# Optimization experiments

Hardware: AMD Instinct MI355X
Metric: run time of the kernel (lower is better)

Reference implementation:

```python
import jax, jax.numpy as jnp
import numpy as np

R = 32          # voxel grid resolution (dense occupancy)
WIN = 8         # window_size
H = 16          # num_heads
C = 1024        # channels
D = C // H      # head_dim = 64
FREQ_DIM = D // 2 // 3   # 10 (3D rope)
ROPE_BASE = 10000.0
EPS_NORM = 1e-12


def setup_inputs() -> dict:
    key = jax.random.key(0)
    ks = jax.random.split(key, 4)
    N = R * R * R
    x = jax.random.normal(ks[0], (N, C), dtype=jnp.float32)
    # dense voxel grid coords in raster (x-major) order, matching token order
    gx, gy, gz = jnp.meshgrid(jnp.arange(R), jnp.arange(R), jnp.arange(R), indexing='ij')
    coords = jnp.stack([gx.reshape(-1), gy.reshape(-1), gz.reshape(-1)], axis=-1).astype(jnp.int32)
    Wqkv = jax.random.normal(ks[1], (C, 3 * C), dtype=jnp.float32) * 0.02
    bqkv = jnp.zeros((3 * C,), dtype=jnp.float32)
    gamma_q = jnp.ones((H, D), dtype=jnp.float32)
    gamma_k = jnp.ones((H, D), dtype=jnp.float32)
    Wout = jax.random.normal(ks[2], (C, C), dtype=jnp.float32) * 0.02
    bout = jnp.zeros((C,), dtype=jnp.float32)
    return {"x": x, "coords": coords, "Wqkv": Wqkv, "bqkv": bqkv,
            "gamma_q": gamma_q, "gamma_k": gamma_k, "Wout": Wout, "bout": bout}


def _mh_rms_norm(t, gamma):
    # SparseMultiHeadRMSNorm: fp32 F.normalize(dim=-1) * gamma * sqrt(D)
    tf = t.astype(jnp.float32)
    norm = jnp.maximum(jnp.sqrt(jnp.sum(tf * tf, axis=-1, keepdims=True)), EPS_NORM)
    return ((tf / norm) * gamma * (D ** 0.5)).astype(t.dtype)


def _rope_cos_sin(coords):
    # freqs: 1.0 / 10000**(i/freq_dim), i in [0, freq_dim)
    freqs = 1.0 / ROPE_BASE ** (jnp.arange(FREQ_DIM, dtype=jnp.float32) / FREQ_DIM)
    phases = coords.astype(jnp.float32)[:, :, None] * freqs  # [N, 3, FREQ_DIM]
    phases = phases.reshape(coords.shape[0], -1)             # [N, 30]
    pad = D // 2 - phases.shape[-1]
    phases = jnp.concatenate([phases, jnp.zeros((coords.shape[0], pad), jnp.float32)], axis=-1)
    return jnp.cos(phases), jnp.sin(phases)                  # [N, D//2] each


def _apply_rope(t, cos, sin):
    # t: [N, H, D] -> pairs [N, H, D//2, 2]; complex mult by (cos + i sin)
    tp = t.reshape(t.shape[0], H, D // 2, 2)
    t0, t1 = tp[..., 0], tp[..., 1]
    c = cos[:, None, :]
    s = sin[:, None, :]
    r0 = t0 * c - t1 * s
    r1 = t0 * s + t1 * c
    return jnp.stack([r0, r1], axis=-1).reshape(t.shape).astype(t.dtype)


def _to_windows(t):
    Rw = R // WIN
    t = t.reshape(Rw, WIN, Rw, WIN, Rw, WIN, H, D)
    t = t.transpose(0, 2, 4, 1, 3, 5, 6, 7)
    return t.reshape(Rw * Rw * Rw, WIN ** 3, H, D)


def _from_windows(t):
    Rw = R // WIN
    t = t.reshape(Rw, Rw, Rw, WIN, WIN, WIN, H, D)
    t = t.transpose(0, 3, 1, 4, 2, 5, 6, 7)
    return t.reshape(R * R * R, H, D)


def reference(x, coords, Wqkv, bqkv, gamma_q, gamma_k, Wout, bout):
    N = x.shape[0]
    qkv = (x @ Wqkv + bqkv).reshape(N, 3, H, D)
    q, k, v = qkv[:, 0], qkv[:, 1], qkv[:, 2]
    # per-head QK RMSNorm (before rope, as in forward)
    q = _mh_rms_norm(q, gamma_q)
    k = _mh_rms_norm(k, gamma_k)
    # inline 3D RoPE from voxel coords
    cos, sin = _rope_cos_sin(coords)
    q = _apply_rope(q, cos, sin)
    k = _apply_rope(k, cos, sin)
    # windowed self-attention (shift_window = (0,0,0), dense grid -> exact partition)
    qw, kw, vw = _to_windows(q), _to_windows(k), _to_windows(v)
    scale = 1.0 / (D ** 0.5)
    scores = jnp.einsum('wqhd,wkhd->whqk', qw, kw) * scale   # [nw, H, T, T]
    attn = jax.nn.softmax(scores, axis=-1)
    hw = jnp.einsum('whqk,wkhd->wqhd', attn, vw)
    h = _from_windows(hw).reshape(N, C)
    return h @ Wout + bout
```

## Files before the change

### kernel.cpp

```cpp
#include <hip/hip_runtime.h>
#include <hip/hip_bf16.h>
#include <stdint.h>

#define DEV static __device__ __forceinline__

typedef __attribute__((ext_vector_type(4))) float f32x4;
typedef __attribute__((ext_vector_type(8))) short s16x8;
typedef __attribute__((ext_vector_type(4))) short s16x4;

constexpr int N_TOK = 32768;
constexpr int C_DIM = 1024;
constexpr int C3    = 3072;
constexpr int GK    = 1024;

DEV float bf2f(short u) { union { float f; uint32_t i; } x; x.i = ((uint32_t)(uint16_t)u) << 16; return x.f; }
DEV short f2bf(float f) { union { float f; uint32_t i; } x; x.f = f; uint32_t r = x.i + 0x7FFFu + ((x.i >> 16) & 1u); return (short)(r >> 16); }

DEV f32x4 mfma16(s16x8 a, s16x8 b, f32x4 c) {
  return __builtin_amdgcn_mfma_f32_16x16x32_bf16(a, b, c, 0, 0, 0);
}

DEV void gload16(const void* g, void* lds) {
  __builtin_amdgcn_global_load_lds((const __attribute__((address_space(1))) void*)g,
                                   (__attribute__((address_space(3))) void*)lds, 16, 0, 0);
}

#define SB() __builtin_amdgcn_sched_barrier(0)
#define WAIT_VM(N) do { asm volatile("s_waitcnt vmcnt(" #N ")" ::: "memory"); SB(); } while (0)
DEV void bar_top() { SB(); __builtin_amdgcn_s_barrier(); asm volatile("s_waitcnt lgkmcnt(0)" ::: "memory"); SB(); }
DEV void bar_end() { SB(); __builtin_amdgcn_s_barrier(); SB(); }

DEV float redsum16(float v) {
  v += __shfl_xor(v, 1); v += __shfl_xor(v, 2); v += __shfl_xor(v, 4); v += __shfl_xor(v, 8);
  return v;
}

__global__ void k_cvt_x(const float* __restrict__ in, short* __restrict__ outb) {
  size_t i = ((size_t)blockIdx.x * 256 + threadIdx.x) * 8;
  float4 a = *(const float4*)(in + i);
  float4 b = *(const float4*)(in + i + 4);
  s16x8 o;
  o[0] = f2bf(a.x); o[1] = f2bf(a.y); o[2] = f2bf(a.z); o[3] = f2bf(a.w);
  o[4] = f2bf(b.x); o[5] = f2bf(b.y); o[6] = f2bf(b.z); o[7] = f2bf(b.w);
  *(s16x8*)(outb + i) = o;
}

__global__ void k_transpose_cvt(const float* __restrict__ in, short* __restrict__ outb,
                                int rin, int cin) {
  __shared__ float t[32][33];
  int tx = threadIdx.x & 31, ty = threadIdx.x >> 5;
  int c0 = blockIdx.x * 32, r0 = blockIdx.y * 32;
#pragma unroll
  for (int k = 0; k < 32; k += 8) t[ty + k][tx] = in[(size_t)(r0 + ty + k) * cin + c0 + tx];
  __syncthreads();
#pragma unroll
  for (int k = 0; k < 32; k += 8) outb[(size_t)(c0 + ty + k) * rin + r0 + tx] = f2bf(t[tx][ty + k]);
}

__global__ void k_ctab(float2* __restrict__ ctab) {
  int t = threadIdx.x;
  if (t >= 320) return;
  int c = t / 10, fi = t % 10;
  float freq = powf(10000.0f, -(float)fi / 10.0f);
  float ph = (float)c * freq;
  ctab[t] = make_float2(cosf(ph), sinf(ph));
}

#define READ_A(b, mh) do { _Pragma("unroll") for (int mi_ = 0; mi_ < 4; ++mi_) \
  _Pragma("unroll") for (int kh_ = 0; kh_ < 2; ++kh_) af[mi_ * 2 + kh_] = LDA(b, (mh) * 4 + mi_, kh_); } while (0)
#define READ_B(b, nh, bfx) do { _Pragma("unroll") for (int ni_ = 0; ni_ < 2; ++ni_) \
  _Pragma("unroll") for (int kh_ = 0; kh_ < 2; ++kh_) (bfx)[ni_ * 2 + kh_] = LDB(b, (nh) * 2 + ni_, kh_); } while (0)
#define MFMAQ(mh, nh, bfx) do { __builtin_amdgcn_s_setprio(1); \
  _Pragma("unroll") for (int mi_ = 0; mi_ < 4; ++mi_) \
  _Pragma("unroll") for (int kh_ = 0; kh_ < 2; ++kh_) \
  _Pragma("unroll") for (int ni_ = 0; ni_ < 2; ++ni_) \
    acc[(mh) * 4 + mi_][(nh) * 2 + ni_] = mfma16(af[mi_ * 2 + kh_], (bfx)[ni_ * 2 + kh_], acc[(mh) * 4 + mi_][(nh) * 2 + ni_]); \
  __builtin_amdgcn_s_setprio(0); } while (0)

DEV void gemm256_core(const short* __restrict__ A, const short* __restrict__ Bt,
                      int tileM, int tileN, short* lds, f32x4 (&acc)[8][4]) {
  const int tid = threadIdx.x;
  const int lane = tid & 63, wid = tid >> 6;
  const int wr = wid >> 2, wc = wid & 3;
  const int g = lane >> 4, r = lane & 15;

#pragma unroll
  for (int mi = 0; mi < 8; ++mi)
#pragma unroll
    for (int ni = 0; ni < 4; ++ni) acc[mi][ni] = (f32x4)0.0f;

  const short* Ag = A + (size_t)tileM * GK;
  const short* Bg = Bt + (size_t)tileN * GK;
  const int ldsA = wr * 8192;
  const int ldsB = 16384 + (wc >> 1) * 8192;
  const int brow = (wc & 1) * 64;

  auto stageA = [&](int b, int h, int kt) {
    const short* gb = Ag + (size_t)(h * 128) * GK + kt * 64;
    short* db = lds + b * 32768 + h * 8192 + (tid & 448) * 8;
#pragma unroll
    for (int i = 0; i < 2; ++i) {
      int s = i * 512 + tid;
      int row = s >> 3;
      int c = (s & 7) ^ (row & 7);
      gload16(gb + (size_t)row * GK + c * 8, db + i * 4096);
    }
  };
  auto stageB = [&](int b, int h, int kt) {
    const short* gb = Bg + (size_t)(h * 128) * GK + kt * 64;
    short* db = lds + b * 32768 + 16384 + h * 8192 + (tid & 448) * 8;
#pragma unroll
    for (int i = 0; i < 2; ++i) {
      int s = i * 512 + tid;
      int row = s >> 3;
      int c = (s & 7) ^ (row & 7);
      gload16(gb + (size_t)row * GK + c * 8, db + i * 4096);
    }
  };
  auto LDA = [&](int b, int mi, int kh) -> s16x8 {
    int row = mi * 16 + r;
    int c = (kh * 4 + g) ^ (r & 7);
    return *(const s16x8*)(lds + b * 32768 + ldsA + row * 64 + c * 8);
  };
  auto LDB = [&](int b, int ni, int kh) -> s16x8 {
    int row = brow + ni * 16 + r;
    int c = (kh * 4 + g) ^ (r & 7);
    return *(const s16x8*)(lds + b * 32768 + ldsB + row * 64 + c * 8);
  };

  s16x8 af[8], bf0[4], bf1[4];

  stageA(0, 0, 0); stageA(0, 1, 0); stageB(0, 0, 0); stageB(0, 1, 0);
  stageB(1, 0, 1); stageB(1, 1, 1);
  WAIT_VM(4);
  __builtin_amdgcn_s_barrier();

#pragma unroll 1
  for (int t = 0; t < 16; t += 2) {
    const bool s2 = (t + 2 < 16), s3 = (t + 3 < 16);
    READ_A(0, 0); READ_B(0, 0, bf0);
    stageA(1, 0, t + 1);
    bar_top(); MFMAQ(0, 0, bf0); bar_end();
    READ_B(0, 1, bf1);
    stageA(1, 1, t + 1);
    bar_top(); MFMAQ(0, 1, bf1); bar_end();
    READ_A(0, 1);
    if (s2) stageB(0, 0, t + 2);
    bar_top(); MFMAQ(1, 0, bf0); bar_end();
    if (s2) stageB(0, 1, t + 2);
    bar_top(); MFMAQ(1, 1, bf1);
    if (s2) { WAIT_VM(4); } else { WAIT_VM(0); }
    bar_end();
    READ_A(1, 0); READ_B(1, 0, bf0);
    if (s2) stageA(0, 0, t + 2);
    bar_top(); MFMAQ(0, 0, bf0); bar_end();
    READ_B(1, 1, bf1);
    if (s2) stageA(0, 1, t + 2);
    bar_top(); MFMAQ(0, 1, bf1); bar_end();
    READ_A(1, 1);
    if (s3) stageB(1, 0, t + 3);
    bar_top(); MFMAQ(1, 0, bf0); bar_end();
    if (s3) stageB(1, 1, t + 3);
    bar_top(); MFMAQ(1, 1, bf1);
    WAIT_VM(4);
    bar_end();
  }
}

__global__ __launch_bounds__(512, 2) void k_gemm_qkv(const short* __restrict__ A, const short* __restrict__ Bt,
                                                     const float* __restrict__ bias,
                                                     const float* __restrict__ gq, const float* __restrict__ gk,
                                                     const float2* __restrict__ ctab,
                                                     short* __restrict__ qw, short* __restrict__ kw,
                                                     short* __restrict__ vw) {
  __shared__ __align__(16) short lds[65536];
  const int nwg = gridDim.x, q8 = nwg >> 3, bid = blockIdx.x;
  const int sb = (bid & 7) * q8 + (bid >> 3);
  const int bx = sb % 12, by = sb / 12;
  const int tileM = by * 256, tileN = bx * 256;
  f32x4 acc[8][4];
  gemm256_core(A, Bt, tileM, tileN, lds, acc);

  const int tid = threadIdx.x, lane = tid & 63, wid = tid >> 6;
  const int wr = wid >> 2, wc = wid & 3, g = lane >> 4, r = lane & 15;
  const int colbase = tileN + wc * 64;
  const int part = colbase >> 10;
  const int head = (colbase >> 6) & 15;
  if (part < 2) {
    __syncthreads();
    float2* ctl = (float2*)lds;
    if (tid < 320) ctl[tid] = ctab[tid];
    __syncthreads();
    short* buf = (part == 0) ? qw : kw;
    const float* gamma = (part == 0) ? gq : gk;
    const float qk_sc = (part == 0) ? 1.4426950408889634f : 8.0f;
    float gam[4];
#pragma unroll
    for (int ni = 0; ni < 4; ++ni) gam[ni] = gamma[head * 64 + ni * 16 + r];
#pragma unroll
    for (int mi = 0; mi < 8; ++mi) {
#pragma unroll
      for (int j = 0; j < 4; ++j) {
        int gr = tileM + wr * 128 + mi * 16 + g * 4 + j;
        int gx = gr >> 10, gy = (gr >> 5) & 31, gz = gr & 31;
        int w = ((gx >> 3) << 4) | ((gy >> 3) << 2) | (gz >> 3);
        int idx = ((gx & 7) << 6) | ((gy & 7) << 3) | (gz & 7);
        int cx = gx, cy = gy, cz = gz;
        size_t base = ((size_t)(w * 16 + head) * 512 + idx) * 64;
        float v[4];
        float ss = 0.f;
#pragma unroll
        for (int ni = 0; ni < 4; ++ni) {
          v[ni] = acc[mi][ni][j] + bias[colbase + ni * 16 + r];
          ss += v[ni] * v[ni];
        }
        ss = redsum16(ss);
        float sc = qk_sc / fmaxf(sqrtf(ss), 1e-12f);
#pragma unroll
        for (int ni = 0; ni < 4; ++ni) v[ni] *= sc * gam[ni];
#pragma unroll
        for (int ni = 0; ni < 4; ++ni) {
          int p = ni * 8 + (r >> 1);
          float c = 1.f, s = 0.f;
          if (p < 30) {
            int axis = (p >= 20) ? 2 : (p >= 10 ? 1 : 0);
            int fi = p - axis * 10;
            int cc = (axis == 0) ? cx : ((axis == 1) ? cy : cz);
            float2 cs = ctl[cc * 10 + fi];
            c = cs.x; s = cs.y;
          }
          float vp = __shfl_xor(v[ni], 1);
          float res = (r & 1) ? (vp * s + v[ni] * c) : (v[ni] * c - vp * s);
          buf[base + ni * 16 + r] = f2bf(res);
        }
      }
    }
  } else {
#pragma unroll
    for (int mi = 0; mi < 8; ++mi) {
#pragma unroll
      for (int j = 0; j < 4; ++j) {
        int gr = tileM + wr * 128 + mi * 16 + g * 4 + j;
        int gx = gr >> 10, gy = (gr >> 5) & 31, gz = gr & 31;
        int w = ((gx >> 3) << 4) | ((gy >> 3) << 2) | (gz >> 3);
        int idx = ((gx & 7) << 6) | ((gy & 7) << 3) | (gz & 7);
        size_t base = (size_t)(w * 16 + head) * 32768 + idx;
#pragma unroll
        for (int ni = 0; ni < 4; ++ni) {
          int d = ni * 16 + r;
          vw[base + (size_t)d * 512] = f2bf(acc[mi][ni][j] + bias[colbase + d]);
        }
      }
    }
  }
}

__global__ __launch_bounds__(512, 2) void k_gemm_out(const short* __restrict__ A, const short* __restrict__ Bt,
                                                     const float* __restrict__ bias, float* __restrict__ out) {
  __shared__ __align__(16) short lds[65536];
  const int nwg = gridDim.x, q8 = nwg >> 3, bid = blockIdx.x;
  const int sb = (bid & 7) * q8 + (bid >> 3);
  const int bx = sb & 3, by = sb >> 2;
  const int tileM = by * 256, tileN = bx * 256;
  f32x4 acc[8][4];
  gemm256_core(A, Bt, tileM, tileN, lds, acc);

  const int tid = threadIdx.x, lane = tid & 63, wid = tid >> 6;
  const int wr = wid >> 2, wc = wid & 3, g = lane >> 4, r = lane & 15;
#pragma unroll
  for (int mi = 0; mi < 8; ++mi)
#pragma unroll
    for (int j = 0; j < 4; ++j) {
      int gr = tileM + wr * 128 + mi * 16 + g * 4 + j;
#pragma unroll
      for (int ni = 0; ni < 4; ++ni) {
        int gc = tileN + wc * 64 + ni * 16 + r;
        out[(size_t)gr * C_DIM + gc] = acc[mi][ni][j] + bias[gc];
      }
    }
}

__global__ __launch_bounds__(256, 2) void k_attn(const short* __restrict__ qw, const short* __restrict__ kw,
                                                 const short* __restrict__ vw, short* __restrict__ hb) {
  __shared__ __align__(16) short Ks[2][4096];
  __shared__ __align__(16) short Vt[2][4096];
  __shared__ __align__(16) short Pb[4][1024];
  const int b = blockIdx.x;
  const int qh = b & 1, head = (b >> 1) & 15, w = b >> 5;
  const int tid = threadIdx.x, lane = tid & 63, wid = tid >> 6;
  const int g = lane >> 4, r = lane & 15;
  const short* Qp = qw + ((size_t)(w * 16 + head) * 512 + qh * 256 + wid * 64) * 64;
  const short* Kp = kw + (size_t)(w * 16 + head) * 32768;
  const short* Vp = vw + (size_t)(w * 16 + head) * 32768;

  s16x8 qf[4][2];
#pragma unroll
  for (int qt = 0; qt < 4; ++qt)
#pragma unroll
    for (int kh = 0; kh < 2; ++kh)
      qf[qt][kh] = *(const s16x8*)(Qp + (qt * 16 + r) * 64 + kh * 32 + g * 8);

  f32x4 o[4][4];
#pragma unroll
  for (int qt = 0; qt < 4; ++qt)
#pragma unroll
    for (int nt = 0; nt < 4; ++nt) o[qt][nt] = (f32x4)0.f;
  float m[4] = {-1e30f, -1e30f, -1e30f, -1e30f};
  float l[4] = {0.f, 0.f, 0.f, 0.f};

  short* PwW = &Pb[wid][0];

  auto stageK = [&](int bufb, int c) {
#pragma unroll
    for (int i = 0; i < 2; ++i) {
      int ci = i * 256 + tid;
      int row = ci >> 3;
      int sc = (ci & 7) ^ (row & 7);
      gload16(Kp + (size_t)(c * 64 + row) * 64 + sc * 8, &Ks[bufb][(i * 256 + (tid & ~63)) * 8]);
    }
  };
  auto stageV = [&](int bufb, int c) {
#pragma unroll
    for (int i = 0; i < 2; ++i) {
      int ci = i * 256 + tid;
      int row = ci >> 3;
      int sc = (ci & 7) ^ (row & 7);
      gload16(Vp + (size_t)row * 512 + c * 64 + sc * 8, &Vt[bufb][(i * 256 + (tid & ~63)) * 8]);
    }
  };

  stageK(0, 0); stageV(0, 0);

#pragma unroll 1
  for (int c = 0; c < 8; ++c) {
    const int cur = c & 1;
    if (c < 7) { stageK(cur ^ 1, c + 1); stageV(cur ^ 1, c + 1); }
    if (c < 7) { WAIT_VM(4); } else { WAIT_VM(0); }
    __builtin_amdgcn_s_barrier();

    s16x8 kf[4][2];
#pragma unroll
    for (int nt = 0; nt < 4; ++nt)
#pragma unroll
      for (int kh = 0; kh < 2; ++kh)
        kf[nt][kh] = *(const s16x8*)(&Ks[cur][0] + (nt * 16 + r) * 64 + (((kh * 4 + g) ^ (r & 7)) << 3));
    s16x8 vfr[4][2];
#pragma unroll
    for (int nt = 0; nt < 4; ++nt)
#pragma unroll
      for (int kh = 0; kh < 2; ++kh)
        vfr[nt][kh] = *(const s16x8*)(&Vt[cur][0] + (nt * 16 + r) * 64 + (((kh * 4 + g) ^ (r & 7)) << 3));

#pragma unroll
    for (int qt = 0; qt < 4; ++qt) {
      f32x4 s4[4];
#pragma unroll
      for (int nt = 0; nt < 4; ++nt) s4[nt] = (f32x4)0.f;
      __builtin_amdgcn_s_setprio(1);
#pragma unroll
      for (int nt = 0; nt < 4; ++nt)
#pragma unroll
        for (int kh = 0; kh < 2; ++kh) s4[nt] = mfma16(kf[nt][kh], qf[qt][kh], s4[nt]);
      __builtin_amdgcn_s_setprio(0);
      float pm = -1e30f;
#pragma unroll
      for (int nt = 0; nt < 4; ++nt)
#pragma unroll
        for (int j = 0; j < 4; ++j) pm = fmaxf(pm, s4[nt][j]);
      pm = fmaxf(pm, __shfl_xor(pm, 16));
      pm = fmaxf(pm, __shfl_xor(pm, 32));
      float mn = fmaxf(m[qt], pm);
      float al = exp2f(m[qt] - mn);
      m[qt] = mn;
      float ps = 0.f;
#pragma unroll
      for (int nt = 0; nt < 4; ++nt)
#pragma unroll
        for (int j = 0; j < 4; ++j) { float p = exp2f(s4[nt][j] - mn); s4[nt][j] = p; ps += p; }
      ps += __shfl_xor(ps, 16);
      ps += __shfl_xor(ps, 32);
      l[qt] = l[qt] * al + ps;
#pragma unroll
      for (int nt = 0; nt < 4; ++nt) o[qt][nt] *= al;
#pragma unroll
      for (int nt = 0; nt < 4; ++nt) {
        uint32_t u0 = (uint32_t)(uint16_t)f2bf(s4[nt][0]) | ((uint32_t)(uint16_t)f2bf(s4[nt][1]) << 16);
        uint32_t u1 = (uint32_t)(uint16_t)f2bf(s4[nt][2]) | ((uint32_t)(uint16_t)f2bf(s4[nt][3]) << 16);
        int col = nt * 16 + g * 4;
        int slot = (col >> 3) ^ (r & 7);
        uint2 uu; uu.x = u0; uu.y = u1;
        *(uint2*)(PwW + r * 64 + slot * 8 + (g & 1) * 4) = uu;
      }
      s16x8 pf0 = *(const s16x8*)(PwW + r * 64 + ((g ^ (r & 7)) << 3));
      s16x8 pf1 = *(const s16x8*)(PwW + r * 64 + (((4 + g) ^ (r & 7)) << 3));
      __builtin_amdgcn_s_setprio(1);
#pragma unroll
      for (int nt = 0; nt < 4; ++nt) {
        o[qt][nt] = mfma16(vfr[nt][0], pf0, o[qt][nt]);
        o[qt][nt] = mfma16(vfr[nt][1], pf1, o[qt][nt]);
      }
      __builtin_amdgcn_s_setprio(0);
    }
    asm volatile("s_waitcnt lgkmcnt(0)" ::: "memory");
    SB();
    __builtin_amdgcn_s_barrier();
  }

#pragma unroll
  for (int qt = 0; qt < 4; ++qt) {
    float inv = 1.f / l[qt];
#pragma unroll
    for (int nt = 0; nt < 4; ++nt) {
      uint32_t u0 = (uint32_t)(uint16_t)f2bf(o[qt][nt][0] * inv) | ((uint32_t)(uint16_t)f2bf(o[qt][nt][1] * inv) << 16);
      uint32_t u1 = (uint32_t)(uint16_t)f2bf(o[qt][nt][2] * inv) | ((uint32_t)(uint16_t)f2bf(o[qt][nt][3] * inv) << 16);
      int col = nt * 16 + g * 4;
      int slot = (col >> 3) ^ (r & 7);
      uint2 uu; uu.x = u0; uu.y = u1;
      *(uint2*)(PwW + r * 64 + slot * 8 + (g & 1) * 4) = uu;
    }
#pragma unroll
    for (int rr = 0; rr < 2; ++rr) {
      int q2 = lane >> 2;
      int cc = (lane & 3) + rr * 4;
      int slot = cc ^ (q2 & 7);
      s16x8 vv = *(const s16x8*)(PwW + q2 * 64 + slot * 8);
      int idx = qh * 256 + wid * 64 + qt * 16 + q2;
      int cx = ((w >> 4) << 3) + (idx >> 6);
      int cy = (((w >> 2) & 3) << 3) + ((idx >> 3) & 7);
      int cz = ((w & 3) << 3) + (idx & 7);
      size_t n = (size_t)cx * 1024 + cy * 32 + cz;
      *(s16x8*)(hb + n * 1024 + head * 64 + cc * 8) = vv;
    }
  }
}

extern "C" void kernel_launch(void* const* d_in, const int* in_sizes, int n_in,
                              void* d_out, int out_size, void* d_ws, size_t ws_size,
                              hipStream_t stream) {
  const float* x    = (const float*)d_in[0];
  const float* Wqkv = (const float*)d_in[2];
  const float* bqkv = (const float*)d_in[3];
  const float* gq   = (const float*)d_in[4];
  const float* gk   = (const float*)d_in[5];
  const float* Wout = (const float*)d_in[6];
  const float* bout = (const float*)d_in[7];
  float* out = (float*)d_out;

  char* ws = (char*)d_ws;
  size_t o = 0;
  auto take = [&](size_t b) { char* p = ws + o; o += (b + 255) & ~(size_t)255; return p; };
  short* xb    = (short*)take((size_t)N_TOK * C_DIM * 2);
  short* wqkvT = (short*)take((size_t)C3 * C_DIM * 2);
  short* woutT = (short*)take((size_t)C_DIM * C_DIM * 2);
  float2* ctab = (float2*)take(320 * sizeof(float2));
  short* qw    = (short*)take((size_t)N_TOK * C_DIM * 2);
  short* kw    = (short*)take((size_t)N_TOK * C_DIM * 2);
  short* vw    = (short*)take((size_t)N_TOK * C_DIM * 2);
  short* hb = xb;

  k_cvt_x<<<(N_TOK * C_DIM) / (256 * 8), 256, 0, stream>>>(x, xb);
  k_transpose_cvt<<<dim3(C3 / 32, C_DIM / 32), 256, 0, stream>>>(Wqkv, wqkvT, C_DIM, C3);
  k_transpose_cvt<<<dim3(C_DIM / 32, C_DIM / 32), 256, 0, stream>>>(Wout, woutT, C_DIM, C_DIM);
  k_ctab<<<1, 320, 0, stream>>>(ctab);
  k_gemm_qkv<<<(C3 / 256) * (N_TOK / 256), 512, 0, stream>>>(xb, wqkvT, bqkv, gq, gk, ctab, qw, kw, vw);
  k_attn<<<2048, 256, 0, stream>>>(qw, kw, vw, hb);
  k_gemm_out<<<(C_DIM / 256) * (N_TOK / 256), 512, 0, stream>>>(hb, woutT, bout, out);
}
```

Baseline: 519.9 us.

## Transpose QKV GEMM epilogue through LDS for vectorized window-layout stores

The QKV GEMM epilogue now stages each wave's accumulator tile through swizzled LDS. For Q/K, each lane holds a full 64-dim head row, so the RMS norm and RoPE run without cross-lane shuffles or reductions, and the row is written with 16-byte stores. For V, values are packed to bf16 in LDS and then written as 8-element vectors into the transposed window layout, replacing scattered 2-byte stores. This trades more per-lane registers (a 64-float row) and LDS traffic, plus RoPE table reads from global memory, for coalesced global writes.

```diff
diff --git a/kernel.cpp b/kernel.cpp
--- a/kernel.cpp
+++ b/kernel.cpp
@@ -186,71 +186,97 @@
   const int colbase = tileN + wc * 64;
   const int part = colbase >> 10;
   const int head = (colbase >> 6) & 15;
+
   if (part < 2) {
-    __syncthreads();
-    float2* ctl = (float2*)lds;
-    if (tid < 320) ctl[tid] = ctab[tid];
-    __syncthreads();
     short* buf = (part == 0) ? qw : kw;
-    const float* gamma = (part == 0) ? gq : gk;
+    const float* gamma = ((part == 0) ? gq : gk) + head * 64;
     const float qk_sc = (part == 0) ? 1.4426950408889634f : 8.0f;
-    float gam[4];
-#pragma unroll
-    for (int ni = 0; ni < 4; ++ni) gam[ni] = gamma[head * 64 + ni * 16 + r];
-#pragma unroll
-    for (int mi = 0; mi < 8; ++mi) {
-#pragma unroll
-      for (int j = 0; j < 4; ++j) {
-        int gr = tileM + wr * 128 + mi * 16 + g * 4 + j;
-        int gx = gr >> 10, gy = (gr >> 5) & 31, gz = gr & 31;
-        int w = ((gx >> 3) << 4) | ((gy >> 3) << 2) | (gz >> 3);
-        int idx = ((gx & 7) << 6) | ((gy & 7) << 3) | (gz & 7);
-        int cx = gx, cy = gy, cz = gz;
-        size_t base = ((size_t)(w * 16 + head) * 512 + idx) * 64;
-        float v[4];
-        float ss = 0.f;
-#pragma unroll
-        for (int ni = 0; ni < 4; ++ni) {
-          v[ni] = acc[mi][ni][j] + bias[colbase + ni * 16 + r];
-          ss += v[ni] * v[ni];
-        }
-        ss = redsum16(ss);
-        float sc = qk_sc / fmaxf(sqrtf(ss), 1e-12f);
-#pragma unroll
-        for (int ni = 0; ni < 4; ++ni) v[ni] *= sc * gam[ni];
-#pragma unroll
-        for (int ni = 0; ni < 4; ++ni) {
-          int p = ni * 8 + (r >> 1);
-          float c = 1.f, s = 0.f;
-          if (p < 30) {
-            int axis = (p >= 20) ? 2 : (p >= 10 ? 1 : 0);
-            int fi = p - axis * 10;
-            int cc = (axis == 0) ? cx : ((axis == 1) ? cy : cz);
-            float2 cs = ctl[cc * 10 + fi];
-            c = cs.x; s = cs.y;
-          }
-          float vp = __shfl_xor(v[ni], 1);
-          float res = (r & 1) ? (vp * s + v[ni] * c) : (v[ni] * c - vp * s);
-          buf[base + ni * 16 + r] = f2bf(res);
-        }
-      }
-    }
-  } else {
-#pragma unroll
-    for (int mi = 0; mi < 8; ++mi) {
-#pragma unroll
-      for (int j = 0; j < 4; ++j) {
-        int gr = tileM + wr * 128 + mi * 16 + g * 4 + j;
-        int gx = gr >> 10, gy = (gr >> 5) & 31, gz = gr & 31;
-        int w = ((gx >> 3) << 4) | ((gy >> 3) << 2) | (gz >> 3);
-        int idx = ((gx & 7) << 6) | ((gy & 7) << 3) | (gz & 7);
-        size_t base = (size_t)(w * 16 + head) * 32768 + idx;
+    float* LW = (float*)lds + wid * 4096;
+#pragma unroll
+    for (int p = 0; p < 2; ++p) {
+#pragma unroll
+      for (int mi_ = 0; mi_ < 4; ++mi_) {
 #pragma unroll
         for (int ni = 0; ni < 4; ++ni) {
           int d = ni * 16 + r;
-          vw[base + (size_t)d * 512] = f2bf(acc[mi][ni][j] + bias[colbase + d]);
+          int c = (mi_ * 4 + g) ^ (d & 15);
+          *(f32x4*)(LW + d * 64 + c * 4) = acc[p * 4 + mi_][ni];
         }
       }
+      float vrow[64];
+#pragma unroll
+      for (int d = 0; d < 64; ++d) {
+        int c = (lane >> 2) ^ (d & 15);
+        vrow[d] = LW[d * 64 + c * 4 + (lane & 3)];
+      }
+      float s0 = 0.f, s1 = 0.f, s2 = 0.f, s3 = 0.f;
+#pragma unroll
+      for (int d = 0; d < 64; d += 4) {
+        vrow[d + 0] += bias[colbase + d + 0];
+        vrow[d + 1] += bias[colbase + d + 1];
+        vrow[d + 2] += bias[colbase + d + 2];
+        vrow[d + 3] += bias[colbase + d + 3];
+        s0 += vrow[d + 0] * vrow[d + 0];
+        s1 += vrow[d + 1] * vrow[d + 1];
+        s2 += vrow[d + 2] * vrow[d + 2];
+        s3 += vrow[d + 3] * vrow[d + 3];
+      }
+      float sc = qk_sc / fmaxf(sqrtf((s0 + s1) + (s2 + s3)), 1e-12f);
+#pragma unroll
+      for (int d = 0; d < 64; ++d) vrow[d] *= sc * gamma[d];
+      int gr = tileM + wr * 128 + p * 64 + lane;
+      int gx = gr >> 10, gy = (gr >> 5) & 31, gz = gr & 31;
+      int w = ((gx >> 3) << 4) | ((gy >> 3) << 2) | (gz >> 3);
+      int idx = ((gx & 7) << 6) | ((gy & 7) << 3) | (gz & 7);
+#pragma unroll
+      for (int a = 0; a < 30; ++a) {
+        int axis = (a < 10) ? 0 : ((a < 20) ? 1 : 2);
+        int fi = a - axis * 10;
+        int cc = (axis == 0) ? gx : ((axis == 1) ? gy : gz);
+        float2 cs = ctab[cc * 10 + fi];
+        float t0 = vrow[2 * a], t1 = vrow[2 * a + 1];
+        vrow[2 * a]     = t0 * cs.x - t1 * cs.y;
+        vrow[2 * a + 1] = t0 * cs.y + t1 * cs.x;
+      }
+      size_t base = ((size_t)(w * 16 + head) * 512 + idx) * 64;
+#pragma unroll
+      for (int k = 0; k < 8; ++k) {
+        s16x8 ov;
+#pragma unroll
+        for (int e = 0; e < 8; ++e) ov[e] = f2bf(vrow[k * 8 + e]);
+        *(s16x8*)(buf + base + k * 8) = ov;
+      }
+    }
+  } else {
+    short* LV = lds + wid * 8192;
+    float bv[4];
+#pragma unroll
+    for (int ni = 0; ni < 4; ++ni) bv[ni] = bias[colbase + ni * 16 + r];
+#pragma unroll
+    for (int mi = 0; mi < 8; ++mi) {
+#pragma unroll
+      for (int ni = 0; ni < 4; ++ni) {
+        int d = ni * 16 + r;
+        int su = (mi * 4 + g) ^ ((d & 7) << 1);
+        uint32_t lo = (uint32_t)(uint16_t)f2bf(acc[mi][ni][0] + bv[ni]) |
+                      ((uint32_t)(uint16_t)f2bf(acc[mi][ni][1] + bv[ni]) << 16);
+        uint32_t hi = (uint32_t)(uint16_t)f2bf(acc[mi][ni][2] + bv[ni]) |
+                      ((uint32_t)(uint16_t)f2bf(acc[mi][ni][3] + bv[ni]) << 16);
+        uint2 uu; uu.x = lo; uu.y = hi;
+        *(uint2*)(LV + d * 128 + su * 4) = uu;
+      }
+    }
+#pragma unroll
+    for (int i = 0; i < 16; ++i) {
+      int d = i * 4 + (lane >> 4);
+      int blk = lane & 15;
+      int su = (2 * blk) ^ ((d & 7) << 1);
+      s16x8 vv = *(const s16x8*)(LV + d * 128 + su * 4);
+      int gr0 = tileM + wr * 128 + blk * 8;
+      int gx = gr0 >> 10, gy = (gr0 >> 5) & 31, gz = gr0 & 31;
+      int w = ((gx >> 3) << 4) | ((gy >> 3) << 2) | (gz >> 3);
+      int idx = ((gx & 7) << 6) | ((gy & 7) << 3);
+      *(s16x8*)(vw + (size_t)(w * 16 + head) * 32768 + (size_t)d * 512 + idx) = vv;
     }
   }
 }
```

New measurement: 639.1 us. 1.23x slower.
